# Kernel tuning notes

Hardware: AMD Instinct MI355X
Metric: run time of the kernel (lower is better)

Reference implementation:

```python
import jax, jax.numpy as jnp
import numpy as np

Q_EPS = 1e-12  # scale clamp used in from_float


def _quantize_rows(w):
    # per-row symmetric int8 quantization: scale = absmax/127, clamp 1e-12
    scales = jnp.clip(jnp.max(jnp.abs(w), axis=1) / 127.0, Q_EPS, None)  # [rows]
    w_i8 = jnp.clip(jnp.round(w / scales[:, None]), -128.0, 127.0)       # int values, fp32 carrier
    return w_i8, scales


def setup_inputs() -> dict:
    key = jax.random.key(0)
    k1, k2, k3 = jax.random.split(key, 3)
    B, S, K, N = 2, 4096, 4096, 4096
    x = jax.random.normal(k1, (B, S, K), dtype=jnp.float32)
    weight_fp = jax.random.normal(k2, (N, K), dtype=jnp.float32) * 0.02
    bias = jax.random.normal(k3, (N,), dtype=jnp.float32) * 0.01
    return {"x": x, "weight_fp": weight_fp, "bias": bias}


def reference(x, weight_fp, bias):
    orig_dtype = x.dtype
    # weight quantization (from_float): per-output-channel scales
    w_i8, w_scales = _quantize_rows(weight_fp)          # [N,K], [N]
    # per-token dynamic activation quantization
    x_shape = x.shape
    x_flat = x.reshape(-1, x_shape[-1])                 # [M,K]
    x_i8, x_scales = _quantize_rows(x_flat)             # [M,K], [M]
    # int8 GEMM accumulated exactly (values fit fp32), fused dequant
    acc = jnp.matmul(x_i8, w_i8.T)                      # [M,N] integer-valued
    out = acc * x_scales[:, None] * w_scales[None, :]
    out = out.astype(jnp.bfloat16)                      # kernel outputs bf16
    out = out.reshape(*x_shape[:-1], w_i8.shape[0])
    out = out + bias.astype(out.dtype)
    return out.astype(orig_dtype)
```

## Files before the change

kernel.cpp:

```cpp
#include <hip/hip_runtime.h>
#include <hip/hip_bf16.h>
#include <stdint.h>


using i32x4 = __attribute__((ext_vector_type(4))) int;

#define TILE 128
#define BK 64

__global__ __launch_bounds__(256) void quant_rows_kernel(
    const float* __restrict__ in, int8_t* __restrict__ qout,
    float* __restrict__ scales, int K)
{
    const int row = blockIdx.x;
    const int tid = threadIdx.x;
    const float* r = in + (size_t)row * K;
    const int base = tid * 16;

    float4 f0 = *(const float4*)(r + base + 0);
    float4 f1 = *(const float4*)(r + base + 4);
    float4 f2 = *(const float4*)(r + base + 8);
    float4 f3 = *(const float4*)(r + base + 12);
    float v[16] = {f0.x,f0.y,f0.z,f0.w, f1.x,f1.y,f1.z,f1.w,
                   f2.x,f2.y,f2.z,f2.w, f3.x,f3.y,f3.z,f3.w};

    float amax = 0.f;
#pragma unroll
    for (int i = 0; i < 16; ++i) amax = fmaxf(amax, fabsf(v[i]));

#pragma unroll
    for (int off = 32; off >= 1; off >>= 1)
        amax = fmaxf(amax, __shfl_xor(amax, off));

    __shared__ float red[4];
    const int wave = tid >> 6;
    if ((tid & 63) == 0) red[wave] = amax;
    __syncthreads();
    amax = fmaxf(fmaxf(red[0], red[1]), fmaxf(red[2], red[3]));

    const float scale = fmaxf(amax / 127.0f, 1e-12f);
    if (tid == 0) scales[row] = scale;

    union { signed char c[16]; i32x4 vec; } u;
#pragma unroll
    for (int i = 0; i < 16; ++i) {
        float q = rintf(v[i] / scale);
        q = fminf(fmaxf(q, -128.f), 127.f);
        u.c[i] = (signed char)(int)q;
    }
    *(i32x4*)(qout + (size_t)row * K + base) = u.vec;
}

__global__ __launch_bounds__(256) void gemm_i8_kernel(
    const int8_t* __restrict__ A,
    const int8_t* __restrict__ B,
    const float*  __restrict__ xs,
    const float*  __restrict__ ws,
    const float*  __restrict__ bias,
    float*        __restrict__ out,
    int M, int N, int K)
{
    __shared__ int8_t sA[TILE * BK];
    __shared__ int8_t sB[TILE * BK];

    const int tid  = threadIdx.x;
    const int wave = tid >> 6;
    const int lane = tid & 63;
    const int quad = lane >> 4;
    const int mrow = lane & 15;

    const int bm = blockIdx.y * TILE;
    const int bn = blockIdx.x * TILE;
    const int wm = (wave >> 1) * 64;
    const int wn = (wave & 1) * 64;

    i32x4 acc[4][4];
    const i32x4 zero = {0, 0, 0, 0};
#pragma unroll
    for (int i = 0; i < 4; ++i)
#pragma unroll
        for (int j = 0; j < 4; ++j) acc[i][j] = zero;

    const int srow = tid >> 2;
    const int soff = (tid & 3) * 16;

    const int8_t* aptr0 = A + (size_t)(bm + srow) * K + soff;
    const int8_t* aptr1 = A + (size_t)(bm + 64 + srow) * K + soff;
    const int8_t* bptr0 = B + (size_t)(bn + srow) * K + soff;
    const int8_t* bptr1 = B + (size_t)(bn + 64 + srow) * K + soff;

    int8_t* sA0 = sA + tid * 16;
    int8_t* sA1 = sA + 4096 + tid * 16;
    int8_t* sB0 = sB + tid * 16;
    int8_t* sB1 = sB + 4096 + tid * 16;

    for (int k0 = 0; k0 < K; k0 += BK) {
        __syncthreads();
        __builtin_amdgcn_global_load_lds(
            (const __attribute__((address_space(1))) void*)(aptr0 + k0),
            (__attribute__((address_space(3))) void*)sA0, 16, 0, 0);
        __builtin_amdgcn_global_load_lds(
            (const __attribute__((address_space(1))) void*)(aptr1 + k0),
            (__attribute__((address_space(3))) void*)sA1, 16, 0, 0);
        __builtin_amdgcn_global_load_lds(
            (const __attribute__((address_space(1))) void*)(bptr0 + k0),
            (__attribute__((address_space(3))) void*)sB0, 16, 0, 0);
        __builtin_amdgcn_global_load_lds(
            (const __attribute__((address_space(1))) void*)(bptr1 + k0),
            (__attribute__((address_space(3))) void*)sB1, 16, 0, 0);
        __syncthreads();

        i32x4 af[4], bfr[4];
#pragma unroll
        for (int i = 0; i < 4; ++i)
            af[i] = *(const i32x4*)(sA + (wm + i * 16 + mrow) * BK + quad * 16);
#pragma unroll
        for (int j = 0; j < 4; ++j)
            bfr[j] = *(const i32x4*)(sB + (wn + j * 16 + mrow) * BK + quad * 16);

#pragma unroll
        for (int i = 0; i < 4; ++i)
#pragma unroll
            for (int j = 0; j < 4; ++j)
                acc[i][j] = __builtin_amdgcn_mfma_i32_16x16x64_i8(
                    af[i], bfr[j], acc[i][j], 0, 0, 0);
    }

#pragma unroll
    for (int j = 0; j < 4; ++j) {
        const int col = bn + wn + j * 16 + mrow;
        const float wsv = ws[col];
        const float bsv = __bfloat162float(__float2bfloat16(bias[col]));
#pragma unroll
        for (int i = 0; i < 4; ++i) {
            const int rowbase = bm + wm + i * 16 + quad * 4;
#pragma unroll
            for (int r = 0; r < 4; ++r) {
                const int row = rowbase + r;
                const float v = (float)acc[i][j][r] * xs[row] * wsv;
                const float vb = __bfloat162float(__float2bfloat16(v));
                const float res = __bfloat162float(__float2bfloat16(vb + bsv));
                out[(size_t)row * N + col] = res;
            }
        }
    }
}

extern "C" void kernel_launch(void* const* d_in, const int* in_sizes, int n_in,
                              void* d_out, int out_size, void* d_ws, size_t ws_size,
                              hipStream_t stream)
{
    const float* x    = (const float*)d_in[0];
    const float* wfp  = (const float*)d_in[1];
    const float* bias = (const float*)d_in[2];
    float* out = (float*)d_out;

    const int N = in_sizes[2];
    const int K = in_sizes[1] / N;
    const int M = in_sizes[0] / K;

    int8_t* w_i8 = (int8_t*)d_ws;
    int8_t* x_i8 = w_i8 + (size_t)N * K;
    float* w_scales = (float*)(x_i8 + (size_t)M * K);
    float* x_scales = w_scales + N;

    quant_rows_kernel<<<N, 256, 0, stream>>>(wfp, w_i8, w_scales, K);
    quant_rows_kernel<<<M, 256, 0, stream>>>(x,   x_i8, x_scales, K);

    dim3 grid(N / TILE, M / TILE);
    gemm_i8_kernel<<<grid, 256, 0, stream>>>(x_i8, w_i8, x_scales, w_scales,
                                             bias, out, M, N, K);
}
```

Baseline: 472.0 us.

## Swizzle LDS tile layout in int8 GEMM and coalesce quantization loads

The GEMM now stores each 16-byte k-chunk of a row at an XOR-like rotated position in shared memory, keyed on row, and the fragment reads use the matching rotation. This is meant to spread the 64-byte-stride fragment reads across LDS banks instead of conflicting. The quantization kernel switches from 16 contiguous floats per thread to four strided float4 loads so each wave's loads and int8 stores are contiguous across lanes. The swizzle must match exactly between the write and read mappings or results break.

```diff
diff --git a/kernel.cpp b/kernel.cpp
--- a/kernel.cpp
+++ b/kernel.cpp
@@ -15,18 +15,20 @@
     const int row = blockIdx.x;
     const int tid = threadIdx.x;
     const float* r = in + (size_t)row * K;
-    const int base = tid * 16;
 
-    float4 f0 = *(const float4*)(r + base + 0);
-    float4 f1 = *(const float4*)(r + base + 4);
-    float4 f2 = *(const float4*)(r + base + 8);
-    float4 f3 = *(const float4*)(r + base + 12);
-    float v[16] = {f0.x,f0.y,f0.z,f0.w, f1.x,f1.y,f1.z,f1.w,
-                   f2.x,f2.y,f2.z,f2.w, f3.x,f3.y,f3.z,f3.w};
+    float4 v[4];
+#pragma unroll
+    for (int j = 0; j < 4; ++j)
+        v[j] = *(const float4*)(r + j * 1024 + tid * 4);
 
     float amax = 0.f;
 #pragma unroll
-    for (int i = 0; i < 16; ++i) amax = fmaxf(amax, fabsf(v[i]));
+    for (int j = 0; j < 4; ++j) {
+        amax = fmaxf(amax, fabsf(v[j].x));
+        amax = fmaxf(amax, fabsf(v[j].y));
+        amax = fmaxf(amax, fabsf(v[j].z));
+        amax = fmaxf(amax, fabsf(v[j].w));
+    }
 
 #pragma unroll
     for (int off = 32; off >= 1; off >>= 1)
@@ -41,14 +43,19 @@
     const float scale = fmaxf(amax / 127.0f, 1e-12f);
     if (tid == 0) scales[row] = scale;
 
-    union { signed char c[16]; i32x4 vec; } u;
 #pragma unroll
-    for (int i = 0; i < 16; ++i) {
-        float q = rintf(v[i] / scale);
-        q = fminf(fmaxf(q, -128.f), 127.f);
-        u.c[i] = (signed char)(int)q;
+    for (int j = 0; j < 4; ++j) {
+        float q0 = fminf(fmaxf(rintf(v[j].x / scale), -128.f), 127.f);
+        float q1 = fminf(fmaxf(rintf(v[j].y / scale), -128.f), 127.f);
+        float q2 = fminf(fmaxf(rintf(v[j].z / scale), -128.f), 127.f);
+        float q3 = fminf(fmaxf(rintf(v[j].w / scale), -128.f), 127.f);
+        union { signed char c[4]; int i; } u;
+        u.c[0] = (signed char)(int)q0;
+        u.c[1] = (signed char)(int)q1;
+        u.c[2] = (signed char)(int)q2;
+        u.c[3] = (signed char)(int)q3;
+        *(int*)(qout + (size_t)row * K + j * 1024 + tid * 4) = u.i;
     }
-    *(i32x4*)(qout + (size_t)row * K + base) = u.vec;
 }
 
 __global__ __launch_bounds__(256) void gemm_i8_kernel(
@@ -82,7 +89,8 @@
         for (int j = 0; j < 4; ++j) acc[i][j] = zero;
 
     const int srow = tid >> 2;
-    const int soff = (tid & 3) * 16;
+    const int g    = ((tid & 3) - ((tid >> 3) & 3)) & 3;
+    const int soff = g * 16;
 
     const int8_t* aptr0 = A + (size_t)(bm + srow) * K + soff;
     const int8_t* aptr1 = A + (size_t)(bm + 64 + srow) * K + soff;
@@ -93,6 +101,8 @@
     int8_t* sA1 = sA + 4096 + tid * 16;
     int8_t* sB0 = sB + tid * 16;
     int8_t* sB1 = sB + 4096 + tid * 16;
+
+    const int rchunk = ((quad + (mrow >> 1)) & 3) * 16;
 
     for (int k0 = 0; k0 < K; k0 += BK) {
         __syncthreads();
@@ -113,10 +123,10 @@
         i32x4 af[4], bfr[4];
 #pragma unroll
         for (int i = 0; i < 4; ++i)
-            af[i] = *(const i32x4*)(sA + (wm + i * 16 + mrow) * BK + quad * 16);
+            af[i] = *(const i32x4*)(sA + (wm + i * 16 + mrow) * BK + rchunk);
 #pragma unroll
         for (int j = 0; j < 4; ++j)
-            bfr[j] = *(const i32x4*)(sB + (wn + j * 16 + mrow) * BK + quad * 16);
+            bfr[j] = *(const i32x4*)(sB + (wn + j * 16 + mrow) * BK + rchunk);
 
 #pragma unroll
         for (int i = 0; i < 4; ++i)
```

Result: no change. 464.5 us (-1.6%).
